# Optimization experiments

Measured on AMD Instinct MI355X. Metric: run time of the kernel, lower is better.

The kernel has to match this reference:

```python
import jax, jax.numpy as jnp
import numpy as np

N, E, G = 25600, 409600, 128   # nodes, edges, graphs
IN, H, C = 200, 4, 64          # raw feat dim, heads, hidden_channels
IN2 = 2 * IN                   # after NaN-mask concat
BN_EPS = 1e-5

def _glorot(key, shape):
    lim = float(np.sqrt(6.0 / (shape[0] + shape[-1])))
    return jax.random.uniform(key, shape, jnp.float32, -lim, lim)

def setup_inputs():
    key = jax.random.key(0)
    k = iter(jax.random.split(key, 40))
    inp = {
        "x": jax.random.normal(next(k), (N, IN), jnp.float32),
        "edge_index": jax.random.randint(next(k), (2, E), 0, N, jnp.int32),
        "edge_attr": jax.random.normal(next(k), (E, 1), jnp.float32),
        "batch": jnp.repeat(jnp.arange(G, dtype=jnp.int32), N // G),
    }
    dims = [(IN2, H, C), (H * C, H, C), (H * C, 1, C)]
    for i, (din, h, c) in enumerate(dims):
        inp[f"W{i}"] = _glorot(next(k), (din, h * c))
        inp[f"as{i}"] = _glorot(next(k), (h, c))
        inp[f"ad{i}"] = _glorot(next(k), (h, c))
        inp[f"We{i}"] = _glorot(next(k), (1, h * c))
        inp[f"ae{i}"] = _glorot(next(k), (h, c))
        inp[f"b{i}"] = jnp.zeros((h * c,), jnp.float32)
    inp["bn_g"] = jnp.ones((H * C,), jnp.float32)
    inp["bn_b"] = jnp.zeros((H * C,), jnp.float32)
    inp["bn_m"] = jnp.zeros((H * C,), jnp.float32)
    inp["bn_v"] = jnp.ones((H * C,), jnp.float32)
    inp["cw1"] = _glorot(next(k), (C, C))
    inp["cb1"] = jnp.zeros((C,), jnp.float32)
    inp["cw2"] = _glorot(next(k), (C, 2))
    inp["cb2"] = jnp.zeros((2,), jnp.float32)
    return inp

def _gat(x, src, dst, ea, W, att_s, att_d, We, att_e, b, heads, ch):
    """PyG GATConv (edge_dim=1, add_self_loops=True, fill_value='mean', concat=True)."""
    n = x.shape[0]
    # self-loop edge_attr = mean of incoming edge_attr per destination node
    cnt = jax.ops.segment_sum(jnp.ones((ea.shape[0], 1), ea.dtype), dst, n)
    loop_ea = jax.ops.segment_sum(ea, dst, n) / jnp.maximum(cnt, 1.0)
    idx = jnp.arange(n, dtype=src.dtype)
    src = jnp.concatenate([src, idx])
    dst = jnp.concatenate([dst, idx])
    ea = jnp.concatenate([ea, loop_ea], axis=0)
    h = (x @ W).reshape(n, heads, ch)                      # [N,H,C]
    a_s = jnp.einsum('nhc,hc->nh', h, att_s)
    a_d = jnp.einsum('nhc,hc->nh', h, att_d)
    a_e = jnp.einsum('ehc,hc->eh', (ea @ We).reshape(-1, heads, ch), att_e)
    alpha = jax.nn.leaky_relu(a_s[src] + a_d[dst] + a_e, 0.2)   # [E',H]
    # segment softmax over destination neighborhoods
    m = jax.ops.segment_max(alpha, dst, n)
    ex = jnp.exp(alpha - m[dst])
    z = jax.ops.segment_sum(ex, dst, n)
    alpha = ex / (z[dst] + 1e-16)
    out = jax.ops.segment_sum(h[src] * alpha[:, :, None], dst, n)  # [N,H,C]
    return out.reshape(n, heads * ch) + b

def reference(x, edge_index, edge_attr, batch,
              W0, as0, ad0, We0, ae0, b0,
              W1, as1, ad1, We1, ae1, b1,
              W2, as2, ad2, We2, ae2, b2,
              bn_g, bn_b, bn_m, bn_v, cw1, cb1, cw2, cb2):
    nan_mask = jnp.isnan(x).astype(x.dtype)
    x = jnp.concatenate([jnp.nan_to_num(x), nan_mask], axis=-1)   # [N, 2*IN]
    edge_attr = jnp.nan_to_num(edge_attr)
    src, dst = edge_index[0], edge_index[1]
    for (W, a_s, a_d, We, a_e, b) in [(W0, as0, ad0, We0, ae0, b0),
                                      (W1, as1, ad1, We1, ae1, b1)]:
        x = _gat(x, src, dst, edge_attr, W, a_s, a_d, We, a_e, b, H, C)
        x = (x - bn_m) / jnp.sqrt(bn_v + BN_EPS) * bn_g + bn_b    # eval-mode BN
        x = jax.nn.relu(x)                                        # dropout = identity (eval)
    x = _gat(x, src, dst, edge_attr, W2, as2, ad2, We2, ae2, b2, 1, C)
    # global mean pool over graphs
    cnt = jax.ops.segment_sum(jnp.ones((x.shape[0], 1), x.dtype), batch, G)
    g = jax.ops.segment_sum(x, batch, G) / jnp.maximum(cnt, 1.0)  # [G, C]
    hdn = jax.nn.gelu(g @ cw1 + cb1, approximate=False)
    return hdn @ cw2 + cb2                                        # [G, 2]
```

## Files before the change

kernel.cpp:

```cpp
#include <hip/hip_runtime.h>
#include <hip/hip_bf16.h>

static const int kN  = 25600;
static const int kE  = 409600;
static const int kG  = 128;
static const int kNPG = 200;
static const int kIN = 200;
static const int kIN2 = 400;
static const int kMD = 64;
#define BN_EPS_ 1e-5f

typedef __attribute__((ext_vector_type(8))) short short8;
typedef __attribute__((ext_vector_type(4))) ushort us4;
typedef __attribute__((ext_vector_type(4))) float f32x4;

__device__ __forceinline__ float bu(ushort u) {
  union { float f; unsigned u32; } x; x.u32 = ((unsigned)u) << 16; return x.f;
}
__device__ __forceinline__ ushort f2u(float v) {
  __hip_bfloat16 t = __float2bfloat16(v);
  return *(ushort*)&t;
}
__device__ __forceinline__ float wredSum(float v) {
#pragma unroll
  for (int off = 1; off < 64; off <<= 1) v += __shfl_xor(v, off, 64);
  return v;
}
__device__ __forceinline__ float lrelu(float a) { return (a > 0.f) ? a : 0.2f * a; }

__global__ void k_pre(const float* __restrict__ x, ushort* __restrict__ x2,
                      const float* __restrict__ W0, ushort* __restrict__ Wt0,
                      const float* __restrict__ W1, ushort* __restrict__ Wt1,
                      const float* __restrict__ W2, ushort* __restrict__ Wt2,
                      const float* __restrict__ We0, const float* __restrict__ ae0,
                      const float* __restrict__ We1, const float* __restrict__ ae1,
                      const float* __restrict__ We2, const float* __restrict__ ae2,
                      float* __restrict__ wed,
                      const int* __restrict__ ei, const float* __restrict__ ea,
                      int2* __restrict__ epk, int* __restrict__ deg) {
  int b = blockIdx.x, tid = threadIdx.x;
  if (b < 5000) {
    int i4 = (b * 256 + tid) * 4;
    int n = i4 / kIN, j = i4 - n * kIN;
    float4 v = *(const float4*)&x[i4];
    ushort o0[4], o1[4];
    float vv[4] = {v.x, v.y, v.z, v.w};
#pragma unroll
    for (int q = 0; q < 4; q++) {
      bool bad = (vv[q] != vv[q]);
      o0[q] = f2u(bad ? 0.f : vv[q]);
      o1[q] = f2u(bad ? 1.f : 0.f);
    }
    *(us4*)&x2[(size_t)n * kIN2 + j] = *(us4*)o0;
    *(us4*)&x2[(size_t)n * kIN2 + kIN + j] = *(us4*)o1;
    return;
  }
  int pb = b - 5000;
  if (pb >= 723) {
    int e = (pb - 723) * 256 + tid;
    int d = ei[kE + e];
    int s = ei[e];
    float v = ea[e];
    if (v != v) v = 0.f;
    int slot = atomicAdd(&deg[d], 1);
    if (slot < kMD) {
      int2 rec; rec.x = s; rec.y = __float_as_int(v);
      epk[(size_t)d * kMD + slot] = rec;
    }
    return;
  }
  if (pb >= 720) {
    int l = pb - 720;
    const float* We = (l == 0) ? We0 : (l == 1) ? We1 : We2;
    const float* ae = (l == 0) ? ae0 : (l == 1) ? ae1 : ae2;
    int n = (l == 2) ? 64 : 256;
    float v = (tid < n) ? We[tid] * ae[tid] : 0.f;
    v = wredSum(v);
    if ((tid & 63) == 0 && tid < n) wed[l * 4 + (tid >> 6)] = v;
    return;
  }
  int i = pb * 256 + tid;
  if (i < 102400) {
    int n = i / kIN2, k = i - n * kIN2;
    Wt0[(size_t)n * kIN2 + k] = f2u(W0[(size_t)k * 256 + n]);
  } else if (i < 102400 + 65536) {
    int j = i - 102400;
    int n = j >> 8, k = j & 255;
    Wt1[(size_t)n * 256 + k] = f2u(W1[(size_t)k * 256 + n]);
  } else {
    int j = i - 102400 - 65536;
    int n = j >> 8, k = j & 255;
    Wt2[(size_t)n * 256 + k] = f2u(W2[(size_t)k * 64 + n]);
  }
}

#define GBK 64
#define GPAD 72

template <int BN, int MT>
__global__ __launch_bounds__(256) void k_gemm_f(const ushort* __restrict__ A,
                                                const ushort* __restrict__ Bt,
                                                ushort* __restrict__ C,
                                                const float* __restrict__ as_g,
                                                const float* __restrict__ ad_g,
                                                float* __restrict__ a_sg,
                                                float* __restrict__ a_dg, int K) {
  constexpr int MI = (BN == 256) ? (MT / 16) : 1;
  constexpr int H = (BN == 256) ? 4 : 1;
  __shared__ ushort As[MT * GPAD];
  __shared__ ushort Bs[BN * GPAD];
  int tid = threadIdx.x;
  int lane = tid & 63, w = tid >> 6;
  int l15 = lane & 15, l4 = lane >> 4;
  int row0 = blockIdx.y * MT;
  int wr = (BN == 256) ? 0 : (w * 16);
  int wc = (BN == 256) ? (w * 64) : 0;
  f32x4 acc[MI][4] = {};
  int ach = tid & 7, arow = tid >> 3;

  for (int kt = 0; kt < K; kt += GBK) {
    __syncthreads();
#pragma unroll
    for (int p = 0; p < MT / 32; p++) {
      int r = p * 32 + arow;
      int kg = kt + ach * 8;
      short8 v = {0, 0, 0, 0, 0, 0, 0, 0};
      if (kg < K) v = *(const short8*)&A[(size_t)(row0 + r) * K + kg];
      *(short8*)&As[r * GPAD + ach * 8] = v;
    }
#pragma unroll
    for (int p = 0; p < BN / 32; p++) {
      int r = p * 32 + arow;
      int kg = kt + ach * 8;
      short8 v = {0, 0, 0, 0, 0, 0, 0, 0};
      if (kg < K) v = *(const short8*)&Bt[(size_t)r * K + kg];
      *(short8*)&Bs[r * GPAD + ach * 8] = v;
    }
    __syncthreads();
#pragma unroll
    for (int kk = 0; kk < 2; kk++) {
      short8 af[MI], bf[4];
#pragma unroll
      for (int mi = 0; mi < MI; mi++)
        af[mi] = *(const short8*)&As[(wr + mi * 16 + l15) * GPAD + kk * 32 + l4 * 8];
#pragma unroll
      for (int ni = 0; ni < 4; ni++)
        bf[ni] = *(const short8*)&Bs[(wc + ni * 16 + l15) * GPAD + kk * 32 + l4 * 8];
#pragma unroll
      for (int mi = 0; mi < MI; mi++)
#pragma unroll
        for (int ni = 0; ni < 4; ni++)
          acc[mi][ni] = __builtin_amdgcn_mfma_f32_16x16x32_bf16(af[mi], bf[ni],
                                                                acc[mi][ni], 0, 0, 0);
    }
  }
#pragma unroll
  for (int mi = 0; mi < MI; mi++) {
    int rbase = row0 + wr + mi * 16 + l4 * 4;
#pragma unroll
    for (int ni = 0; ni < 4; ni++) {
      int col = wc + ni * 16 + l15;
#pragma unroll
      for (int r = 0; r < 4; r++)
        C[(size_t)(rbase + r) * BN + col] = f2u(acc[mi][ni][r]);
    }
  }
  float asv[4], adv[4];
#pragma unroll
  for (int ni = 0; ni < 4; ni++) {
    asv[ni] = as_g[wc + ni * 16 + l15];
    adv[ni] = ad_g[wc + ni * 16 + l15];
  }
  int hh = (BN == 256) ? w : 0;
#pragma unroll
  for (int mi = 0; mi < MI; mi++) {
#pragma unroll
    for (int r = 0; r < 4; r++) {
      float ps = 0.f, pd = 0.f;
#pragma unroll
      for (int ni = 0; ni < 4; ni++) {
        ps += acc[mi][ni][r] * asv[ni];
        pd += acc[mi][ni][r] * adv[ni];
      }
#pragma unroll
      for (int off = 1; off < 16; off <<= 1) {
        ps += __shfl_xor(ps, off, 64);
        pd += __shfl_xor(pd, off, 64);
      }
      if (l15 == 0) {
        int row = row0 + wr + mi * 16 + l4 * 4 + r;
        a_sg[row * H + hh] = ps;
        a_dg[row * H + hh] = pd;
      }
    }
  }
}

__global__ __launch_bounds__(256) void k_agg4(
    const ushort* __restrict__ hbuf, const int2* __restrict__ epk,
    const int* __restrict__ deg, const float* __restrict__ a_s,
    const float* __restrict__ a_d, const float* __restrict__ wed,
    const float* __restrict__ bias, const float* __restrict__ bng,
    const float* __restrict__ bnb, const float* __restrict__ bnm,
    const float* __restrict__ bnv, ushort* __restrict__ xout) {
  int tid = threadIdx.x;
  int w = tid >> 6, lane = tid & 63;
  int d = blockIdx.x * 4 + w;
  const int2* rp = &epk[(size_t)d * kMD];
  int dgt = deg[d];
  int dg = min(dgt, kMD);
  int h = lane >> 4;
  float adh = a_d[d * 4 + h];
  float wdh = wed[h];

  int c0 = lane * 4;
  float a0 = 0.f, a1 = 0.f, a2 = 0.f, a3 = 0.f, sz = 0.f, sea = 0.f;
  int k = 0;
  for (; k + 8 <= dg; k += 8) {
    int2 r[8];
#pragma unroll
    for (int j = 0; j < 8; j++) r[j] = rp[k + j];
    ushort4 v8[8];
    float s8[8];
#pragma unroll
    for (int j = 0; j < 8; j++) {
      v8[j] = *(const ushort4*)&hbuf[(size_t)r[j].x * 256 + c0];
      s8[j] = a_s[r[j].x * 4 + h];
    }
#pragma unroll
    for (int j = 0; j < 8; j++) {
      float e0 = __int_as_float(r[j].y);
      float ww = __expf(lrelu(s8[j] + adh + e0 * wdh));
      sea += e0;
      sz += ww;
      a0 += ww * bu(v8[j].x); a1 += ww * bu(v8[j].y);
      a2 += ww * bu(v8[j].z); a3 += ww * bu(v8[j].w);
    }
  }
  for (; k < dg; k++) {
    int2 r0 = rp[k];
    float e0 = __int_as_float(r0.y);
    ushort4 v0 = *(const ushort4*)&hbuf[(size_t)r0.x * 256 + c0];
    float w0 = __expf(lrelu(a_s[r0.x * 4 + h] + adh + e0 * wdh));
    sea += e0;
    sz += w0;
    a0 += w0 * bu(v0.x); a1 += w0 * bu(v0.y);
    a2 += w0 * bu(v0.z); a3 += w0 * bu(v0.w);
  }
  {
    float lea = sea / fmaxf((float)dgt, 1.f);
    ushort4 v0 = *(const ushort4*)&hbuf[(size_t)d * 256 + c0];
    float w0 = __expf(lrelu(a_s[d * 4 + h] + adh + lea * wdh));
    sz += w0;
    a0 += w0 * bu(v0.x); a1 += w0 * bu(v0.y);
    a2 += w0 * bu(v0.z); a3 += w0 * bu(v0.w);
  }
  float winv = 1.f / (sz + 1e-16f);

  float4 bi = *(const float4*)&bias[c0];
  a0 = a0 * winv + bi.x; a1 = a1 * winv + bi.y;
  a2 = a2 * winv + bi.z; a3 = a3 * winv + bi.w;
  float4 g4 = *(const float4*)&bng[c0], b4 = *(const float4*)&bnb[c0];
  float4 m4 = *(const float4*)&bnm[c0], v4 = *(const float4*)&bnv[c0];
  a0 = fmaxf((a0 - m4.x) * rsqrtf(v4.x + BN_EPS_) * g4.x + b4.x, 0.f);
  a1 = fmaxf((a1 - m4.y) * rsqrtf(v4.y + BN_EPS_) * g4.y + b4.y, 0.f);
  a2 = fmaxf((a2 - m4.z) * rsqrtf(v4.z + BN_EPS_) * g4.z + b4.z, 0.f);
  a3 = fmaxf((a3 - m4.w) * rsqrtf(v4.w + BN_EPS_) * g4.w + b4.w, 0.f);
  ushort4 o = make_ushort4(f2u(a0), f2u(a1), f2u(a2), f2u(a3));
  *(ushort4*)&xout[(size_t)d * 256 + c0] = o;
}

__global__ __launch_bounds__(256) void k_agg1(
    const ushort* __restrict__ hbuf, const int2* __restrict__ epk,
    const int* __restrict__ deg, const float* __restrict__ a_s,
    const float* __restrict__ a_d, const float* __restrict__ wed,
    const float* __restrict__ bias, float* __restrict__ xout) {
  int tid = threadIdx.x;
  int w = tid >> 6, lane = tid & 63;
  int d = blockIdx.x * 4 + w;
  const int2* rp = &epk[(size_t)d * kMD];
  int dgt = deg[d];
  int dg = min(dgt, kMD);
  float adh = a_d[d];
  float wdh = wed[0];

  float acc = 0.f, sz = 0.f, sea = 0.f;
  int k = 0;
  for (; k + 8 <= dg; k += 8) {
    int2 r[8];
#pragma unroll
    for (int j = 0; j < 8; j++) r[j] = rp[k + j];
    ushort v8[8];
    float s8[8];
#pragma unroll
    for (int j = 0; j < 8; j++) {
      v8[j] = hbuf[(size_t)r[j].x * 64 + lane];
      s8[j] = a_s[r[j].x];
    }
#pragma unroll
    for (int j = 0; j < 8; j++) {
      float e0 = __int_as_float(r[j].y);
      float ww = __expf(lrelu(s8[j] + adh + e0 * wdh));
      sea += e0;
      sz += ww;
      acc += ww * bu(v8[j]);
    }
  }
  for (; k < dg; k++) {
    int2 r0 = rp[k];
    float e0 = __int_as_float(r0.y);
    float w0 = __expf(lrelu(a_s[r0.x] + adh + e0 * wdh));
    sea += e0;
    sz += w0;
    acc += w0 * bu(hbuf[(size_t)r0.x * 64 + lane]);
  }
  {
    float lea = sea / fmaxf((float)dgt, 1.f);
    float w0 = __expf(lrelu(a_s[d] + adh + lea * wdh));
    sz += w0;
    acc += w0 * bu(hbuf[(size_t)d * 64 + lane]);
  }
  acc = acc / (sz + 1e-16f) + bias[lane];
  xout[(size_t)d * 64 + lane] = acc;
}

__global__ void k_poolhead(const float* __restrict__ xin,
                           const float* __restrict__ cw1, const float* __restrict__ cb1,
                           const float* __restrict__ cw2, const float* __restrict__ cb2,
                           float* __restrict__ out) {
  __shared__ float part[4][64];
  __shared__ float gb[64], hb[64];
  int g = blockIdx.x, tid = threadIdx.x;
  int c = tid & 63, w = tid >> 6;
  float acc = 0.f;
  size_t base = (size_t)g * kNPG * 64;
  for (int n = w; n < kNPG; n += 4) acc += xin[base + (size_t)n * 64 + c];
  part[w][c] = acc;
  __syncthreads();
  if (tid < 64) {
    float s = (part[0][c] + part[1][c]) + (part[2][c] + part[3][c]);
    gb[c] = s * (1.f / kNPG);
  }
  __syncthreads();
  if (tid < 64) {
    float s = cb1[c];
#pragma unroll 8
    for (int i = 0; i < 64; i++) s += gb[i] * cw1[i * 64 + c];
    s = 0.5f * s * (1.f + erff(s * 0.70710678118654752f));
    hb[c] = s;
  }
  __syncthreads();
  if (tid < 2) {
    float o = cb2[tid];
    for (int i = 0; i < 64; i++) o += hb[i] * cw2[i * 2 + tid];
    out[g * 2 + tid] = o;
  }
}


extern "C" void kernel_launch(void* const* d_in, const int* in_sizes, int n_in,
                              void* d_out, int out_size, void* d_ws, size_t ws_size,
                              hipStream_t stream) {
  (void)in_sizes; (void)n_in; (void)out_size; (void)ws_size;
  const float* x  = (const float*)d_in[0];
  const int* ei   = (const int*)d_in[1];
  const float* ea = (const float*)d_in[2];
  const float *W[3], *as_[3], *ad_[3], *We[3], *ae[3], *bi[3];
  for (int l = 0; l < 3; l++) {
    W[l]   = (const float*)d_in[4 + l * 6 + 0];
    as_[l] = (const float*)d_in[4 + l * 6 + 1];
    ad_[l] = (const float*)d_in[4 + l * 6 + 2];
    We[l]  = (const float*)d_in[4 + l * 6 + 3];
    ae[l]  = (const float*)d_in[4 + l * 6 + 4];
    bi[l]  = (const float*)d_in[4 + l * 6 + 5];
  }
  const float* bng = (const float*)d_in[22];
  const float* bnb = (const float*)d_in[23];
  const float* bnm = (const float*)d_in[24];
  const float* bnv = (const float*)d_in[25];
  const float* cw1 = (const float*)d_in[26];
  const float* cb1 = (const float*)d_in[27];
  const float* cw2 = (const float*)d_in[28];
  const float* cb2 = (const float*)d_in[29];

  char* p = (char*)d_ws;
  auto alloc = [&](size_t bytes) -> void* {
    void* r = (void*)p;
    p += (bytes + 255) & ~(size_t)255;
    return r;
  };
  ushort* x2b   = (ushort*)alloc((size_t)kN * kIN2 * 2);
  ushort* hbufb = (ushort*)alloc((size_t)kN * 256 * 2);
  ushort* xbA   = (ushort*)alloc((size_t)kN * 256 * 2);
  ushort* xbB   = (ushort*)alloc((size_t)kN * 256 * 2);
  float*  fbuf  = (float*)alloc((size_t)kN * 64 * 4);
  ushort* Wt0   = (ushort*)alloc((size_t)kIN2 * 256 * 2);
  ushort* Wt1   = (ushort*)alloc((size_t)256 * 256 * 2);
  ushort* Wt2   = (ushort*)alloc((size_t)256 * 64 * 2);
  float* a_s    = (float*)alloc((size_t)kN * 4 * 4);
  float* a_d    = (float*)alloc((size_t)kN * 4 * 4);
  int2* epk     = (int2*)alloc((size_t)kN * kMD * 8);
  float* wed    = (float*)alloc(256);
  int* deg      = (int*)alloc((size_t)kN * 4);

  hipMemsetAsync(deg, 0, (size_t)kN * 4, stream);
  k_pre<<<5000 + 720 + 3 + 1600, 256, 0, stream>>>(
      x, x2b, W[0], Wt0, W[1], Wt1, W[2], Wt2, We[0], ae[0], We[1], ae[1],
      We[2], ae[2], wed, ei, ea, epk, deg);
  dim3 gg64m(1, kN / 64);
  k_gemm_f<256, 64><<<gg64m, 256, 0, stream>>>(x2b, Wt0, hbufb, as_[0], ad_[0],
                                               a_s, a_d, kIN2);
  k_agg4<<<kN / 4, 256, 0, stream>>>(hbufb, epk, deg, a_s, a_d,
                                     &wed[0], bi[0], bng, bnb, bnm, bnv, xbA);
  k_gemm_f<256, 64><<<gg64m, 256, 0, stream>>>(xbA, Wt1, hbufb, as_[1], ad_[1],
                                               a_s, a_d, 256);
  k_agg4<<<kN / 4, 256, 0, stream>>>(hbufb, epk, deg, a_s, a_d,
                                     &wed[4], bi[1], bng, bnb, bnm, bnv, xbB);
  dim3 gg64(1, kN / 64);
  k_gemm_f<64, 64><<<gg64, 256, 0, stream>>>(xbB, Wt2, hbufb, as_[2], ad_[2],
                                             a_s, a_d, 256);
  k_agg1<<<kN / 4, 256, 0, stream>>>(hbufb, epk, deg, a_s, a_d,
                                     &wed[8], bi[2], fbuf);
  k_poolhead<<<kG, 256, 0, stream>>>(fbuf, cw1, cb1, cw2, cb2, (float*)d_out);
}
```

Baseline: 323.7 us.

## Precompute per-edge attention weights once per wave into LDS before aggregation

The aggregation kernels used to have every lane recompute the exp/leaky-relu attention weight for every edge, redundant across the 16 lanes of a head. Now the kernels first spread edges across lanes, compute each edge/head weight once, and store the weights and source indices in shared memory. Softmax sums and the mean self-loop edge attribute come from wave shuffle reductions. The gather loop then only reads weights from LDS, which cuts redundant exp and a_s gathers at the cost of extra LDS traffic and a reduction step. No barrier separates the LDS writes from the reads, which relies on each wave using only its own LDS slice.

```diff
diff --git a/kernel.cpp b/kernel.cpp
--- a/kernel.cpp
+++ b/kernel.cpp
@@ -203,59 +203,83 @@
     const float* __restrict__ bias, const float* __restrict__ bng,
     const float* __restrict__ bnb, const float* __restrict__ bnm,
     const float* __restrict__ bnv, ushort* __restrict__ xout) {
+  __shared__ float lds_w[4][kMD][4];
+  __shared__ int   lds_s[4][kMD];
+  __shared__ float lds_m[4][4][2];
   int tid = threadIdx.x;
   int w = tid >> 6, lane = tid & 63;
   int d = blockIdx.x * 4 + w;
   const int2* rp = &epk[(size_t)d * kMD];
   int dgt = deg[d];
   int dg = min(dgt, kMD);
-  int h = lane >> 4;
-  float adh = a_d[d * 4 + h];
-  float wdh = wed[h];
-
+
+  int h1 = lane & 3, slot0 = lane >> 2;
+  float adh1 = a_d[d * 4 + h1];
+  float wdh1 = wed[h1];
+  float szp = 0.f, seap = 0.f;
+  for (int t = 0; t < dg; t += 16) {
+    int slot = t + slot0;
+    float wv = 0.f, ev = 0.f;
+    if (slot < dg) {
+      int2 rec = rp[slot];
+      ev = __int_as_float(rec.y);
+      float asv = a_s[rec.x * 4 + h1];
+      wv = __expf(lrelu(asv + adh1 + ev * wdh1));
+      lds_w[w][slot][h1] = wv;
+      if (h1 == 0) lds_s[w][slot] = rec.x;
+    }
+    szp += wv;
+    seap += (h1 == 0) ? ev : 0.f;
+  }
+#pragma unroll
+  for (int off = 4; off < 64; off <<= 1) {
+    szp  += __shfl_xor(szp, off, 64);
+    seap += __shfl_xor(seap, off, 64);
+  }
+  float sea = __shfl(seap, lane & 0x3C, 64);
+  float lea = sea / fmaxf((float)dgt, 1.f);
+  float selfw1 = __expf(lrelu(a_s[d * 4 + h1] + adh1 + lea * wdh1));
+  float szh = szp + selfw1;
+  if (slot0 == 0) {
+    lds_m[w][h1][0] = 1.f / (szh + 1e-16f);
+    lds_m[w][h1][1] = selfw1;
+  }
+
+  int h2 = lane >> 4;
   int c0 = lane * 4;
-  float a0 = 0.f, a1 = 0.f, a2 = 0.f, a3 = 0.f, sz = 0.f, sea = 0.f;
+  float a0 = 0.f, a1 = 0.f, a2 = 0.f, a3 = 0.f;
   int k = 0;
   for (; k + 8 <= dg; k += 8) {
-    int2 r[8];
-#pragma unroll
-    for (int j = 0; j < 8; j++) r[j] = rp[k + j];
+    int s8[8]; float w8[8];
+#pragma unroll
+    for (int j = 0; j < 8; j++) {
+      s8[j] = lds_s[w][k + j];
+      w8[j] = lds_w[w][k + j][h2];
+    }
     ushort4 v8[8];
-    float s8[8];
+#pragma unroll
+    for (int j = 0; j < 8; j++)
+      v8[j] = *(const ushort4*)&hbuf[(size_t)s8[j] * 256 + c0];
 #pragma unroll
     for (int j = 0; j < 8; j++) {
-      v8[j] = *(const ushort4*)&hbuf[(size_t)r[j].x * 256 + c0];
-      s8[j] = a_s[r[j].x * 4 + h];
-    }
-#pragma unroll
-    for (int j = 0; j < 8; j++) {
-      float e0 = __int_as_float(r[j].y);
-      float ww = __expf(lrelu(s8[j] + adh + e0 * wdh));
-      sea += e0;
-      sz += ww;
-      a0 += ww * bu(v8[j].x); a1 += ww * bu(v8[j].y);
-      a2 += ww * bu(v8[j].z); a3 += ww * bu(v8[j].w);
+      a0 += w8[j] * bu(v8[j].x); a1 += w8[j] * bu(v8[j].y);
+      a2 += w8[j] * bu(v8[j].z); a3 += w8[j] * bu(v8[j].w);
     }
   }
   for (; k < dg; k++) {
-    int2 r0 = rp[k];
-    float e0 = __int_as_float(r0.y);
-    ushort4 v0 = *(const ushort4*)&hbuf[(size_t)r0.x * 256 + c0];
-    float w0 = __expf(lrelu(a_s[r0.x * 4 + h] + adh + e0 * wdh));
-    sea += e0;
-    sz += w0;
+    int s0 = lds_s[w][k];
+    float w0 = lds_w[w][k][h2];
+    ushort4 v0 = *(const ushort4*)&hbuf[(size_t)s0 * 256 + c0];
     a0 += w0 * bu(v0.x); a1 += w0 * bu(v0.y);
     a2 += w0 * bu(v0.z); a3 += w0 * bu(v0.w);
   }
+  float winv = lds_m[w][h2][0];
+  float sw   = lds_m[w][h2][1];
   {
-    float lea = sea / fmaxf((float)dgt, 1.f);
     ushort4 v0 = *(const ushort4*)&hbuf[(size_t)d * 256 + c0];
-    float w0 = __expf(lrelu(a_s[d * 4 + h] + adh + lea * wdh));
-    sz += w0;
-    a0 += w0 * bu(v0.x); a1 += w0 * bu(v0.y);
-    a2 += w0 * bu(v0.z); a3 += w0 * bu(v0.w);
-  }
-  float winv = 1.f / (sz + 1e-16f);
+    a0 += sw * bu(v0.x); a1 += sw * bu(v0.y);
+    a2 += sw * bu(v0.z); a3 += sw * bu(v0.w);
+  }
 
   float4 bi = *(const float4*)&bias[c0];
   a0 = a0 * winv + bi.x; a1 = a1 * winv + bi.y;
@@ -275,6 +299,8 @@
     const int* __restrict__ deg, const float* __restrict__ a_s,
     const float* __restrict__ a_d, const float* __restrict__ wed,
     const float* __restrict__ bias, float* __restrict__ xout) {
+  __shared__ float lds_w[4][kMD];
+  __shared__ int   lds_s[4][kMD];
   int tid = threadIdx.x;
   int w = tid >> 6, lane = tid & 63;
   int d = blockIdx.x * 4 + w;
@@ -284,43 +310,44 @@
   float adh = a_d[d];
   float wdh = wed[0];
 
-  float acc = 0.f, sz = 0.f, sea = 0.f;
+  float wv = 0.f, ev = 0.f;
+  if (lane < dg) {
+    int2 rec = rp[lane];
+    ev = __int_as_float(rec.y);
+    wv = __expf(lrelu(a_s[rec.x] + adh + ev * wdh));
+    lds_w[w][lane] = wv;
+    lds_s[w][lane] = rec.x;
+  }
+  float szp = wv, seap = ev;
+#pragma unroll
+  for (int off = 1; off < 64; off <<= 1) {
+    szp  += __shfl_xor(szp, off, 64);
+    seap += __shfl_xor(seap, off, 64);
+  }
+  float lea = seap / fmaxf((float)dgt, 1.f);
+  float selfw = __expf(lrelu(a_s[d] + adh + lea * wdh));
+  float winv = 1.f / (szp + selfw + 1e-16f);
+
+  float acc = 0.f;
   int k = 0;
   for (; k + 8 <= dg; k += 8) {
-    int2 r[8];
-#pragma unroll
-    for (int j = 0; j < 8; j++) r[j] = rp[k + j];
+    int s8[8]; float w8[8];
+#pragma unroll
+    for (int j = 0; j < 8; j++) {
+      s8[j] = lds_s[w][k + j];
+      w8[j] = lds_w[w][k + j];
+    }
     ushort v8[8];
-    float s8[8];
-#pragma unroll
-    for (int j = 0; j < 8; j++) {
-      v8[j] = hbuf[(size_t)r[j].x * 64 + lane];
-      s8[j] = a_s[r[j].x];
-    }
-#pragma unroll
-    for (int j = 0; j < 8; j++) {
-      float e0 = __int_as_float(r[j].y);
-      float ww = __expf(lrelu(s8[j] + adh + e0 * wdh));
-      sea += e0;
-      sz += ww;
-      acc += ww * bu(v8[j]);
-    }
+#pragma unroll
+    for (int j = 0; j < 8; j++) v8[j] = hbuf[(size_t)s8[j] * 64 + lane];
+#pragma unroll
+    for (int j = 0; j < 8; j++) acc += w8[j] * bu(v8[j]);
   }
   for (; k < dg; k++) {
-    int2 r0 = rp[k];
-    float e0 = __int_as_float(r0.y);
-    float w0 = __expf(lrelu(a_s[r0.x] + adh + e0 * wdh));
-    sea += e0;
-    sz += w0;
-    acc += w0 * bu(hbuf[(size_t)r0.x * 64 + lane]);
-  }
-  {
-    float lea = sea / fmaxf((float)dgt, 1.f);
-    float w0 = __expf(lrelu(a_s[d] + adh + lea * wdh));
-    sz += w0;
-    acc += w0 * bu(hbuf[(size_t)d * 64 + lane]);
-  }
-  acc = acc / (sz + 1e-16f) + bias[lane];
+    acc += lds_w[w][k] * bu(hbuf[(size_t)lds_s[w][k] * 64 + lane]);
+  }
+  acc += selfw * bu(hbuf[(size_t)d * 64 + lane]);
+  acc = acc * winv + bias[lane];
   xout[(size_t)d * 64 + lane] = acc;
 }
 
```

Result: faster. 299.3 us (-7.5%).
